# Kernel optimization log

Hardware: AMD Instinct MI355X
Metric: run time of the kernel (lower is better)

The kernel has to match this reference:

```python
import jax, jax.numpy as jnp
import numpy as np

B, F, U, O, A, H = 8192, 1024, 512, 3, 6, 4  # batch, features, nb_units, nb_opponents, actions, heads
HD = U // H  # head dim


def setup_inputs() -> dict:
    key = jax.random.key(0)
    ks = jax.random.split(key, 12)
    s = 0.02
    rn = lambda k, shape: jax.random.normal(k, shape, jnp.float32) * s
    return {
        "features": jax.random.normal(ks[0], (B, F), jnp.float32),
        # agent latent Linear
        "W_al": rn(ks[1], (U, F)), "b_al": jnp.zeros((U,), jnp.float32),
        # MultiheadAttention in_proj (q,k,v stacked) and out_proj
        "W_in": rn(ks[2], (3 * U, U)), "b_in": jnp.zeros((3 * U,), jnp.float32),
        "W_out": rn(ks[3], (U, U)), "b_out": jnp.zeros((U,), jnp.float32),
        # agent head / policy / value
        "W_ah": rn(ks[4], (U, 2 * U)), "b_ah": jnp.zeros((U,), jnp.float32),
        "W_ap": rn(ks[5], (A, U)), "b_ap": jnp.zeros((A,), jnp.float32),
        "W_av": rn(ks[6], (1, U)), "b_av": jnp.zeros((1,), jnp.float32),
        # per-opponent stacks: latent, head, policy, value
        "W_ol": rn(ks[7], (O, U, F)), "b_ol": jnp.zeros((O, U), jnp.float32),
        "W_oh": rn(ks[8], (O, U, U)), "b_oh": jnp.zeros((O, U), jnp.float32),
        "W_op": rn(ks[9], (O, A, U)), "b_op": jnp.zeros((O, A), jnp.float32),
        "W_ov": rn(ks[10], (O, 1, U)), "b_ov": jnp.zeros((O, 1), jnp.float32),
    }


def reference(features, W_al, b_al, W_in, b_in, W_out, b_out, W_ah, b_ah,
              W_ap, b_ap, W_av, b_av, W_ol, b_ol, W_oh, b_oh, W_op, b_op, W_ov, b_ov):
    elu = jax.nn.elu
    # agent + per-opponent latents (per-opponent linears as one grouped GEMM)
    agent_latent = elu(features @ W_al.T + b_al)                                # [B,U]
    opp_lat = elu(jnp.einsum('bf,ouf->obu', features, W_ol) + b_ol[:, None, :])  # [O,B,U]

    # torch.nn.MultiheadAttention: query=[1,B,U] (agent), key=value=[O,B,U] (opponents)
    Wq, Wk, Wv = W_in[:U], W_in[U:2 * U], W_in[2 * U:]
    bq, bk, bv = b_in[:U], b_in[U:2 * U], b_in[2 * U:]
    q = (agent_latent @ Wq.T + bq).reshape(B, H, HD) * (1.0 / np.sqrt(HD))      # [B,H,HD]
    k = (jnp.einsum('obu,vu->obv', opp_lat, Wk) + bk).reshape(O, B, H, HD)
    v = (jnp.einsum('obu,vu->obv', opp_lat, Wv) + bv).reshape(O, B, H, HD)
    scores = jnp.einsum('bhd,obhd->bho', q, k)                                  # [B,H,O]
    w = jax.nn.softmax(scores, axis=-1)
    attn = jnp.einsum('bho,obhd->bhd', w, v).reshape(B, U)
    attn_out = attn @ W_out.T + b_out                                           # [B,U]
    opponents_influences = w.mean(axis=1)                                       # [B,O] (avg over heads)

    # agent head / policy / value
    cat = jnp.concatenate([agent_latent, attn_out], axis=1)                     # [B,2U]
    agent_head = elu(cat @ W_ah.T + b_ah)
    agent_policy = agent_head @ W_ap.T + b_ap                                   # [B,A]
    agent_value = agent_head @ W_av.T + b_av                                    # [B,1]

    # per-opponent head / policy / value (grouped GEMMs)
    opp_heads = elu(jnp.einsum('obu,ovu->obv', opp_lat, W_oh) + b_oh[:, None, :])  # [O,B,U]
    opponents_policies = jnp.einsum('obu,oau->boa', opp_heads, W_op) + b_op[None]   # [B,O,A]
    opponents_values = jnp.einsum('obu,ocu->boc', opp_heads, W_ov) + b_ov[None]     # [B,O,1]

    return (agent_policy, agent_value, opponents_policies, opponents_values, opponents_influences)
```

## Files before the change

### kernel.cpp

```cpp
#include <hip/hip_runtime.h>

typedef unsigned short u16;
typedef __bf16 bf16x8 __attribute__((ext_vector_type(8)));
typedef float f32x4 __attribute__((ext_vector_type(4)));

#define Bsz 8192
#define Fdim 1024
#define Udim 512
#define Odim 3
#define Adim 6
#define Hdim 4

#define OFF_FEAT   0
#define OFF_WAL    8388608
#define OFF_WIN    10485760
#define OFF_WOUT   11272192
#define OFF_WAH    11534336
#define OFF_WOH    12058624
#define OFF_LAT    12845056
#define OFF_Q      29622272
#define OFF_KV     33816576
#define OFF_ATT    58982400
#define OFF_AGH    63176704
#define OFF_OPH    67371008
#define OFF_WOUTT  79953920
#define OFF_WCOMB  80216064
#define OFF_BAHC   80478208
#define OFF_ZB     80479232

#define OUT_AP 0
#define OUT_AV 49152
#define OUT_OP 57344
#define OUT_OV 204800
#define OUT_IN 229376

__device__ __forceinline__ u16 f2bf(float f) {
  return __builtin_bit_cast(u16, (__bf16)f);
}
__device__ __forceinline__ float bf2f(u16 u) {
  return (float)__builtin_bit_cast(__bf16, u);
}

__device__ __forceinline__ void gload16(const u16* g, u16* s) {
  __builtin_amdgcn_global_load_lds(
      (const __attribute__((address_space(1))) unsigned int*)g,
      (__attribute__((address_space(3))) unsigned int*)s, 16, 0, 0);
}

#define CV_E0 2097152
#define CV_E1 2228224
#define CV_E2 2621440
#define CV_E3 2818048
#define CV_E4 2883584
#define CV_E5 3014656
#define CV_E6 3211264
__global__ __launch_bounds__(256) void convert_all(
    const float* __restrict__ f, const float* __restrict__ wal,
    const float* __restrict__ wol, const float* __restrict__ win,
    const float* __restrict__ wout, const float* __restrict__ wah,
    const float* __restrict__ woh, u16* __restrict__ dst,
    u16* __restrict__ woutT, float* __restrict__ bahc,
    const float* __restrict__ bout_f, const float* __restrict__ bah_f,
    float* __restrict__ zb) {
  if (blockIdx.x >= 12608) {
    const int wave = threadIdx.x >> 6, lane = threadIdx.x & 63;
    const int jbase = (blockIdx.x - 12608) * 8 + wave * 2;
#pragma unroll
    for (int t = 0; t < 2; ++t) {
      const int j = jbase + t;
      float s = 0.f;
#pragma unroll
      for (int c = 0; c < 8; ++c)
        s += wah[j * 1024 + 512 + c * 64 + lane] * bout_f[c * 64 + lane];
#pragma unroll
      for (int d = 32; d; d >>= 1) s += __shfl_xor(s, d, 64);
      if (lane == 0) bahc[j] = bah_f[j] + s;
    }
    return;
  }
  if (blockIdx.x >= 12544) {
    const int bid = blockIdx.x - 12544;
    if (bid == 0) {
      zb[threadIdx.x] = 0.f;
      zb[threadIdx.x + 256] = 0.f;
    }
    __shared__ float tile[64][65];
    const int bx = bid & 7, byy = bid >> 3;
    const int v0 = byy * 64, u0 = bx * 64;
#pragma unroll
    for (int it = 0; it < 16; ++it) {
      int idx = it * 256 + threadIdx.x;
      int r = idx >> 6, c = idx & 63;
      tile[r][c] = wout[(v0 + r) * 512 + u0 + c];
    }
    __syncthreads();
#pragma unroll
    for (int it = 0; it < 16; ++it) {
      int idx = it * 256 + threadIdx.x;
      int r = idx >> 6, c = idx & 63;
      woutT[(u0 + r) * 512 + v0 + c] = f2bf(tile[c][r]);
    }
    return;
  }
  int i = blockIdx.x * 256 + threadIdx.x;
  const float* src;
  int base;
  if (i < CV_E0)      { src = f;    base = 0; }
  else if (i < CV_E1) { src = wal;  base = CV_E0; }
  else if (i < CV_E2) { src = wol;  base = CV_E1; }
  else if (i < CV_E3) { src = win;  base = CV_E2; }
  else if (i < CV_E4) { src = wout; base = CV_E3; }
  else if (i < CV_E5) { src = wah;  base = CV_E4; }
  else                { src = woh;  base = CV_E5; }
  float4 v = ((const float4*)src)[i - base];
  ushort4 o;
  o.x = f2bf(v.x); o.y = f2bf(v.y); o.z = f2bf(v.z); o.w = f2bf(v.w);
  ((ushort4*)dst)[i] = o;
}

#define BAR() __builtin_amdgcn_s_barrier()
#define FENCE() asm volatile("" ::: "memory")
#define LGKM0() asm volatile("s_waitcnt lgkmcnt(0)" ::: "memory")
#define VMW(n) asm volatile("s_waitcnt vmcnt(" #n ")" ::: "memory")
#define MFMA(a, b, c) __builtin_amdgcn_mfma_f32_16x16x32_bf16(a, b, c, 0, 0, 0)
#define STAGE(MAT, SRC, LD, buf, ks, kb) do {                    \
    const u16* _s = (SRC) + (size_t)(kb) + (ks) * 32;            \
    gload16(_s, &MAT[buf][ks][wave * 512]);                      \
    gload16(_s + (size_t)128 * (LD), &MAT[buf][ks][4096 + wave * 512]); \
  } while (0)
#define RD_A(cur, ks, mh) do {                                   \
    _Pragma("unroll")                                            \
    for (int mi = 0; mi < 4; mi++)                               \
      a0[mi] = *(const bf16x8*)&As[cur][ks][aoff + (mh)*2048 + mi*512]; \
  } while (0)
#define RD_B(cur, ks) do {                                       \
    _Pragma("unroll")                                            \
    for (int ni = 0; ni < 4; ni++)                               \
      b0[ni] = *(const bf16x8*)&Bs[cur][ks][boff + ni*512];      \
  } while (0)
#define MFMA8(mh) do {                                           \
    __builtin_amdgcn_s_setprio(1);                               \
    _Pragma("unroll")                                            \
    for (int mi = 0; mi < 4; mi++) {                             \
      _Pragma("unroll")                                          \
      for (int ni = 0; ni < 4; ni++)                             \
        acc[(mh)*4+mi][ni] = MFMA(a0[mi], b0[ni], acc[(mh)*4+mi][ni]); \
    }                                                            \
    __builtin_amdgcn_s_setprio(0);                               \
  } while (0)

template <bool ELU>
__global__ __launch_bounds__(512, 2) void gemm256(
    const u16* __restrict__ A, const u16* __restrict__ Bw, u16* __restrict__ C,
    const float* __restrict__ bias1, const float* __restrict__ bias2,
    int bsplit, int K, int lda, int ldb, int ldc,
    long sAz, long sBz, long sCz, int sbz, float scale) {
  __shared__ __align__(16) u16 As[2][2][8192];
  __shared__ __align__(16) u16 Bs[2][2][8192];
  const int tid = threadIdx.x;
  const int wave = tid >> 6, lane = tid & 63;
  const int wr = wave >> 2, wc = wave & 3;

  const int nx = gridDim.x, ny = gridDim.y;
  const int nxy = nx * ny;
  const int nwg = nxy * gridDim.z;
  const int orig = blockIdx.x + nx * (blockIdx.y + ny * blockIdx.z);
  const int xcd = orig & 7;
  const int qd = nwg >> 3, rd = nwg & 7;
  const int wg = (xcd < rd ? xcd * (qd + 1) : rd * (qd + 1) + (xcd - rd) * qd)
               + (orig >> 3);
  const int z = wg / nxy;
  const int rem = wg - z * nxy;
  const int by = rem / nx;
  const int bx = rem - by * nx;

  A += (size_t)z * sAz;
  Bw += (size_t)z * sBz;
  C += (size_t)z * sCz;
  bias1 += (size_t)z * sbz;

  const int tM = by * 256, tN = bx * 256;

  const int srow = tid >> 2;
  const int schunk = ((tid & 3) ^ ((tid >> 3) & 3)) * 8;
  const u16* Asrc = A + (size_t)(tM + srow) * lda + schunk;
  const u16* Bsrc = Bw + (size_t)(tN + srow) * ldb + schunk;

  const int laneLo = lane & 15;
  const int pc8 = (((lane >> 4) ^ ((lane >> 1) & 3))) * 8;
  const int aoff = (wr * 128 + laneLo) * 32 + pc8;
  const int boff = (wc * 64 + laneLo) * 32 + pc8;

  f32x4 acc[8][4];
#pragma unroll
  for (int mi = 0; mi < 8; mi++)
#pragma unroll
    for (int ni = 0; ni < 4; ni++) acc[mi][ni] = (f32x4){0.f, 0.f, 0.f, 0.f};

  const int NT = K >> 6;

  STAGE(As, Asrc, lda, 0, 0, 0);
  STAGE(Bs, Bsrc, ldb, 0, 0, 0);
  STAGE(As, Asrc, lda, 0, 1, 0);
  STAGE(Bs, Bsrc, ldb, 0, 1, 0);
  VMW(4);
  BAR();

  int cur = 0;
  int kb = 64;
  bf16x8 a0[4], b0[4];
  for (int t = 0; t < NT; ++t) {
    const int nxt = cur ^ 1;
    const bool st = (t + 1 < NT);
    RD_B(cur, 0);
    RD_A(cur, 0, 0);
    if (st) STAGE(As, Asrc, lda, nxt, 0, kb);
    FENCE(); BAR(); LGKM0();
    MFMA8(0);
    FENCE(); BAR();
    RD_A(cur, 0, 1);
    if (st) STAGE(Bs, Bsrc, ldb, nxt, 0, kb);
    FENCE(); BAR(); LGKM0();
    MFMA8(1);
    if (st) { VMW(4); } else { VMW(0); }
    BAR();
    RD_B(cur, 1);
    RD_A(cur, 1, 0);
    if (st) STAGE(As, Asrc, lda, nxt, 1, kb);
    FENCE(); BAR(); LGKM0();
    MFMA8(0);
    FENCE(); BAR();
    RD_A(cur, 1, 1);
    if (st) STAGE(Bs, Bsrc, ldb, nxt, 1, kb);
    FENCE(); BAR(); LGKM0();
    MFMA8(1);
    if (st) { VMW(4); BAR(); }
    cur = nxt;
    kb += 64;
  }

#pragma unroll
  for (int ni = 0; ni < 4; ni++) {
    const int col = tN + wc * 64 + ni * 16 + laneLo;
    const float bv = (col < bsplit) ? bias1[col] : bias2[col - bsplit];
#pragma unroll
    for (int gm = 0; gm < 8; gm++) {
      const int row0 = tM + wr * 128 + gm * 16 + (lane >> 4) * 4;
#pragma unroll
      for (int r = 0; r < 4; r++) {
        float v = (acc[gm][ni][r] + bv) * scale;
        if (ELU) v = v > 0.f ? v : (__expf(v) - 1.f);
        C[(size_t)(row0 + r) * ldc + col] = f2bf(v);
      }
    }
  }
}
#undef STAGE
#undef RD_A
#undef RD_B
#undef MFMA8

template <int BN, bool ELU>
__global__ __launch_bounds__(256) void gemm_bt(
    const u16* __restrict__ A, const u16* __restrict__ A2,
    const u16* __restrict__ Bw, const u16* __restrict__ Bw2,
    int ksplit, int lda, int lda2, int ldb, int ldb2,
    u16* __restrict__ C, const float* __restrict__ bias,
    int K, int ldc, float scale) {
  constexpr int BM = 128, BK = 32;
  constexpr int NI = BN / 32;
  __shared__ __align__(16) u16 As[BM * BK];
  __shared__ __align__(16) u16 Bs[BN * BK];
  const int wave = threadIdx.x >> 6, lane = threadIdx.x & 63;

  const int nx = gridDim.x;
  const int nwg = nx * gridDim.y;
  const int orig = blockIdx.x + nx * blockIdx.y;
  const int xcd = orig & 7;
  const int qd = nwg >> 3, rd = nwg & 7;
  const int wg = (xcd < rd ? xcd * (qd + 1) : rd * (qd + 1) + (xcd - rd) * qd)
               + (orig >> 3);
  const int by = wg / nx, bx = wg - by * nx;
  const int tM = by * BM, tN = bx * BN;
  const int wr = wave >> 1, wc = wave & 1;

  f32x4 acc[4][NI];
#pragma unroll
  for (int i = 0; i < 4; i++)
#pragma unroll
    for (int j = 0; j < NI; j++) acc[i][j] = (f32x4){0.f, 0.f, 0.f, 0.f};

  const int srow = lane >> 2;
  const int scol = (lane & 3) * 8;

  for (int k0 = 0; k0 < K; k0 += BK) {
    const u16 *Ap, *Bp;
    int la, lb, kk;
    if (k0 < ksplit) { Ap = A;  la = lda;  Bp = Bw;  lb = ldb;  kk = k0; }
    else             { Ap = A2; la = lda2; Bp = Bw2; lb = ldb2; kk = k0 - ksplit; }
    __syncthreads();
#pragma unroll
    for (int i = 0; i < 2; ++i) {
      int r = wave * 32 + i * 16;
      gload16(Ap + (size_t)(tM + r + srow) * la + kk + scol, &As[r * BK]);
    }
#pragma unroll
    for (int i = 0; i < BN / 64; ++i) {
      int r = (wave * (BN / 64) + i) * 16;
      gload16(Bp + (size_t)(tN + r + srow) * lb + kk + scol, &Bs[r * BK]);
    }
    __syncthreads();
    bf16x8 af[4], bfr[NI];
#pragma unroll
    for (int mi = 0; mi < 4; mi++)
      af[mi] = *(const bf16x8*)&As[(wr * 64 + mi * 16 + (lane & 15)) * BK + (lane >> 4) * 8];
#pragma unroll
    for (int ni = 0; ni < NI; ni++)
      bfr[ni] = *(const bf16x8*)&Bs[(wc * (BN / 2) + ni * 16 + (lane & 15)) * BK + (lane >> 4) * 8];
#pragma unroll
    for (int mi = 0; mi < 4; mi++)
#pragma unroll
      for (int ni = 0; ni < NI; ni++)
        acc[mi][ni] = __builtin_amdgcn_mfma_f32_16x16x32_bf16(af[mi], bfr[ni], acc[mi][ni], 0, 0, 0);
  }

#pragma unroll
  for (int ni = 0; ni < NI; ni++) {
    int col = tN + wc * (BN / 2) + ni * 16 + (lane & 15);
    float bv = bias[col];
#pragma unroll
    for (int mi = 0; mi < 4; mi++) {
      int row0 = tM + wr * 64 + mi * 16 + (lane >> 4) * 4;
#pragma unroll
      for (int r = 0; r < 4; r++) {
        float v = (acc[mi][ni][r] + bv) * scale;
        if (ELU) v = v > 0.f ? v : (__expf(v) - 1.f);
        C[(size_t)(row0 + r) * ldc + col] = f2bf(v);
      }
    }
  }
}

__global__ __launch_bounds__(256) void mega(
    const u16* __restrict__ lat, const u16* __restrict__ win,
    const u16* __restrict__ woh, const u16* __restrict__ wahb,
    const u16* __restrict__ woutT,
    u16* __restrict__ qb, u16* __restrict__ kvb, u16* __restrict__ oph,
    u16* __restrict__ wcomb,
    const float* __restrict__ b_in, const float* __restrict__ b_oh,
    const float* __restrict__ zb) {
  constexpr int BM = 128, BK = 32, BN = 128, NI = 4;
  __shared__ __align__(16) u16 As[BM * BK];
  __shared__ __align__(16) u16 Bs[BN * BK];
  const int wave = threadIdx.x >> 6, lane = threadIdx.x & 63;

  const int orig = blockIdx.x;
  const int wg = (orig & 7) * 322 + (orig >> 3);

  const u16 *A, *Bw;
  u16* C;
  const float* bias;
  int bx, by, ldc, lda = 2048;
  bool elu = false;
  float scale = 1.f;
  if (wg < 256) {
    bx = wg & 3; by = wg >> 2;
    A = lat; Bw = win; C = qb; bias = b_in;
    ldc = 512; scale = 0.08838834764831845f;
  } else if (wg < 1792) {
    int t = wg - 256, o = t >> 9, r = t & 511;
    bx = r & 7; by = r >> 3;
    A = lat + 512 * (o + 1); Bw = win + 262144;
    C = kvb + (size_t)o * 8388608; bias = b_in + 512;
    ldc = 1024;
  } else if (wg < 2560) {
    int t = wg - 1792, o = t >> 8, r = t & 255;
    bx = r & 3; by = r >> 2;
    A = lat + 512 * (o + 1); Bw = woh + (size_t)o * 262144;
    C = oph + (size_t)o * 4194304; bias = b_oh + o * 512;
    ldc = 512; elu = true;
  } else {
    int t = wg - 2560;
    bx = t & 3; by = t >> 2;
    A = wahb + 512; lda = 1024; Bw = woutT;
    C = wcomb; bias = zb;
    ldc = 512;
  }
  const int tM = by * BM, tN = bx * BN;
  const int wr = wave >> 1, wc = wave & 1;

  f32x4 acc[4][NI];
#pragma unroll
  for (int i = 0; i < 4; i++)
#pragma unroll
    for (int j = 0; j < NI; j++) acc[i][j] = (f32x4){0.f, 0.f, 0.f, 0.f};

  const int srow = lane >> 2;
  const int scol = (lane & 3) * 8;

  for (int k0 = 0; k0 < 512; k0 += BK) {
    __syncthreads();
#pragma unroll
    for (int i = 0; i < 2; ++i) {
      int r = wave * 32 + i * 16;
      gload16(A + (size_t)(tM + r + srow) * lda + k0 + scol, &As[r * BK]);
    }
#pragma unroll
    for (int i = 0; i < 2; ++i) {
      int r = (wave * 2 + i) * 16;
      gload16(Bw + (size_t)(tN + r + srow) * 512 + k0 + scol, &Bs[r * BK]);
    }
    __syncthreads();
    bf16x8 af[4], bfr[NI];
#pragma unroll
    for (int mi = 0; mi < 4; mi++)
      af[mi] = *(const bf16x8*)&As[(wr * 64 + mi * 16 + (lane & 15)) * BK + (lane >> 4) * 8];
#pragma unroll
    for (int ni = 0; ni < NI; ni++)
      bfr[ni] = *(const bf16x8*)&Bs[(wc * 64 + ni * 16 + (lane & 15)) * BK + (lane >> 4) * 8];
#pragma unroll
    for (int mi = 0; mi < 4; mi++)
#pragma unroll
      for (int ni = 0; ni < NI; ni++)
        acc[mi][ni] = __builtin_amdgcn_mfma_f32_16x16x32_bf16(af[mi], bfr[ni], acc[mi][ni], 0, 0, 0);
  }

#pragma unroll
  for (int ni = 0; ni < NI; ni++) {
    int col = tN + wc * 64 + ni * 16 + (lane & 15);
    float bv = bias[col];
#pragma unroll
    for (int mi = 0; mi < 4; mi++) {
      int row0 = tM + wr * 64 + mi * 16 + (lane >> 4) * 4;
#pragma unroll
      for (int r = 0; r < 4; r++) {
        float v = (acc[mi][ni][r] + bv) * scale;
        if (elu) v = v > 0.f ? v : (__expf(v) - 1.f);
        C[(size_t)(row0 + r) * ldc + col] = f2bf(v);
      }
    }
  }
}

__global__ __launch_bounds__(256) void attn_kernel(
    const u16* __restrict__ q, const u16* __restrict__ kv,
    u16* __restrict__ attn, float* __restrict__ influ) {
  const int wave = threadIdx.x >> 6, lane = threadIdx.x & 63;
  const int b = blockIdx.x * 4 + wave;
  const size_t qb = (size_t)b * 512;
  float wacc0 = 0.f, wacc1 = 0.f, wacc2 = 0.f;
#pragma unroll
  for (int h = 0; h < 4; ++h) {
    const int off = h * 128 + lane * 2;
    ushort2 qu = *(const ushort2*)(q + qb + off);
    float qx = bf2f(qu.x), qy = bf2f(qu.y);
    float s[3];
#pragma unroll
    for (int o = 0; o < 3; ++o) {
      ushort2 ku = *(const ushort2*)(kv + (size_t)o * (Bsz * 1024) + (size_t)b * 1024 + off);
      float p = qx * bf2f(ku.x) + qy * bf2f(ku.y);
#pragma unroll
      for (int d = 32; d; d >>= 1) p += __shfl_xor(p, d, 64);
      s[o] = p;
    }
    float m = fmaxf(s[0], fmaxf(s[1], s[2]));
    float e0 = __expf(s[0] - m), e1 = __expf(s[1] - m), e2 = __expf(s[2] - m);
    float inv = 1.f / (e0 + e1 + e2);
    float w0 = e0 * inv, w1 = e1 * inv, w2 = e2 * inv;
    wacc0 += w0; wacc1 += w1; wacc2 += w2;
    float ax = 0.f, ay = 0.f;
#pragma unroll
    for (int o = 0; o < 3; ++o) {
      float w = (o == 0) ? w0 : (o == 1) ? w1 : w2;
      ushort2 vu = *(const ushort2*)(kv + (size_t)o * (Bsz * 1024) + (size_t)b * 1024 + 512 + off);
      ax += w * bf2f(vu.x);
      ay += w * bf2f(vu.y);
    }
    ushort2 st; st.x = f2bf(ax); st.y = f2bf(ay);
    *(ushort2*)(attn + qb + off) = st;
  }
  if (lane == 0) {
    influ[b * 3 + 0] = wacc0 * 0.25f;
    influ[b * 3 + 1] = wacc1 * 0.25f;
    influ[b * 3 + 2] = wacc2 * 0.25f;
  }
}

__global__ __launch_bounds__(256) void heads_kernel(
    const u16* __restrict__ ah, const u16* __restrict__ oh,
    const float* __restrict__ Wap, const float* __restrict__ bap,
    const float* __restrict__ Wav, const float* __restrict__ bav,
    const float* __restrict__ Wop, const float* __restrict__ bop,
    const float* __restrict__ Wov, const float* __restrict__ bov,
    float* __restrict__ out) {
  __shared__ float sW[14336];
  for (int i = threadIdx.x; i < 14336; i += 256) {
    int s = i / 3584, rem = i - s * 3584;
    float v;
    if (s == 0) {
      v = (rem < 3072) ? Wap[rem] : Wav[rem - 3072];
    } else {
      int o = s - 1;
      v = (rem < 3072) ? Wop[o * 3072 + rem] : Wov[o * 512 + (rem - 3072)];
    }
    sW[i] = v;
  }
  __syncthreads();
  const int wave = threadIdx.x >> 6, lane = threadIdx.x & 63;
  const int kq = lane & 7, r = lane >> 3;
  const int b = blockIdx.x * 32 + wave * 8 + r;

  const u16* srcs[4] = {ah + (size_t)b * 512,
                        oh + (size_t)b * 512,
                        oh + (size_t)(Bsz + b) * 512,
                        oh + (size_t)(2 * Bsz + b) * 512};
  bf16x8 a[4][8];
#pragma unroll
  for (int s = 0; s < 4; s++)
#pragma unroll
    for (int c = 0; c < 8; c++)
      a[s][c] = *(const bf16x8*)(srcs[s] + c * 64 + kq * 8);

#pragma unroll
  for (int s = 0; s < 4; s++) {
#pragma unroll
    for (int p = 0; p < 7; p++) {
      const float* w = &sW[s * 3584 + p * 512 + kq * 8];
      float acc = 0.f;
#pragma unroll
      for (int c = 0; c < 8; c++) {
#pragma unroll
        for (int j = 0; j < 8; j++)
          acc += (float)a[s][c][j] * w[c * 64 + j];
      }
      acc += __shfl_xor(acc, 1, 64);
      acc += __shfl_xor(acc, 2, 64);
      acc += __shfl_xor(acc, 4, 64);
      if (kq == p) {
        if (s == 0) {
          if (p < 6) out[OUT_AP + b * 6 + p] = acc + bap[p];
          else       out[OUT_AV + b] = acc + bav[0];
        } else {
          int o = s - 1;
          if (p < 6) out[OUT_OP + b * 18 + o * 6 + p] = acc + bop[o * 6 + p];
          else       out[OUT_OV + b * 3 + o] = acc + bov[o];
        }
      }
    }
  }
}

extern "C" void kernel_launch(void* const* d_in, const int* in_sizes, int n_in,
                              void* d_out, int out_size, void* d_ws, size_t ws_size,
                              hipStream_t stream) {
  (void)in_sizes; (void)n_in; (void)out_size; (void)ws_size;
  const float* f     = (const float*)d_in[0];
  const float* W_al  = (const float*)d_in[1];
  const float* b_al  = (const float*)d_in[2];
  const float* W_in  = (const float*)d_in[3];
  const float* b_in  = (const float*)d_in[4];
  const float* W_out = (const float*)d_in[5];
  const float* b_out = (const float*)d_in[6];
  const float* W_ah  = (const float*)d_in[7];
  const float* b_ah  = (const float*)d_in[8];
  const float* W_ap  = (const float*)d_in[9];
  const float* b_ap  = (const float*)d_in[10];
  const float* W_av  = (const float*)d_in[11];
  const float* b_av  = (const float*)d_in[12];
  const float* W_ol  = (const float*)d_in[13];
  const float* b_ol  = (const float*)d_in[14];
  const float* W_oh  = (const float*)d_in[15];
  const float* b_oh  = (const float*)d_in[16];
  const float* W_op  = (const float*)d_in[17];
  const float* b_op  = (const float*)d_in[18];
  const float* W_ov  = (const float*)d_in[19];
  const float* b_ov  = (const float*)d_in[20];
  float* out = (float*)d_out;
  u16* ws = (u16*)d_ws;

  u16* feat  = ws + OFF_FEAT;
  u16* wal   = ws + OFF_WAL;
  u16* win   = ws + OFF_WIN;
  u16* wahb  = ws + OFF_WAH;
  u16* woh   = ws + OFF_WOH;
  u16* lat   = ws + OFF_LAT;
  u16* qb    = ws + OFF_Q;
  u16* kvb   = ws + OFF_KV;
  u16* att   = ws + OFF_ATT;
  u16* agh   = ws + OFF_AGH;
  u16* oph   = ws + OFF_OPH;
  u16* woutT = ws + OFF_WOUTT;
  u16* wcomb = ws + OFF_WCOMB;
  float* bahc = (float*)(ws + OFF_BAHC);
  float* zb   = (float*)(ws + OFF_ZB);

  convert_all<<<12672, 256, 0, stream>>>(f, W_al, W_ol, W_in, W_out, W_ah,
                                         W_oh, ws, woutT, bahc, b_out, b_ah,
                                         zb);

  gemm256<true><<<dim3(8, 32, 1), 512, 0, stream>>>(
      feat, wal, lat, b_al, b_ol, 512, 1024, 1024, 1024, 2048, 0, 0, 0, 0, 1.f);

  mega<<<2576, 256, 0, stream>>>(
      lat, win, woh, wahb, woutT, qb, kvb, oph, wcomb, b_in, b_oh, zb);

  attn_kernel<<<2048, 256, 0, stream>>>(qb, kvb, att, out + OUT_IN);

  gemm_bt<64, true><<<dim3(8, 64), 256, 0, stream>>>(
      lat, att, wahb, wcomb, 512, 2048, 512, 1024, 512,
      agh, bahc, 1024, 512, 1.f);

  heads_kernel<<<256, 256, 0, stream>>>(agh, oph, W_ap, b_ap, W_av, b_av,
                                        W_op, b_op, W_ov, b_ov, out);
}
```

Baseline: 290.9 us.

## Fuse attention, agent-head GEMM and policy/value heads into one tail kernel

Replaces the attention kernel, the agent-head GEMM and the heads kernel with a single tail kernel that handles 32 batch rows per 512-thread block. Attention output and agent latent stay in swizzled LDS, and the agent head result is written back to LDS and consumed directly by the policy/value dot products. This drops the global round trips for the attn and agent_head buffers and two kernel launches. In exchange only 256 blocks run, each with a serial 32-step K loop and no double buffering. Head weights are read from global fp32 instead of being staged in LDS.

```diff
diff --git a/kernel.cpp b/kernel.cpp
--- a/kernel.cpp
+++ b/kernel.cpp
@@ -20,8 +20,6 @@
 #define OFF_LAT    12845056
 #define OFF_Q      29622272
 #define OFF_KV     33816576
-#define OFF_ATT    58982400
-#define OFF_AGH    63176704
 #define OFF_OPH    67371008
 #define OFF_WOUTT  79953920
 #define OFF_WCOMB  80216064
@@ -260,87 +258,6 @@
 #undef RD_B
 #undef MFMA8
 
-template <int BN, bool ELU>
-__global__ __launch_bounds__(256) void gemm_bt(
-    const u16* __restrict__ A, const u16* __restrict__ A2,
-    const u16* __restrict__ Bw, const u16* __restrict__ Bw2,
-    int ksplit, int lda, int lda2, int ldb, int ldb2,
-    u16* __restrict__ C, const float* __restrict__ bias,
-    int K, int ldc, float scale) {
-  constexpr int BM = 128, BK = 32;
-  constexpr int NI = BN / 32;
-  __shared__ __align__(16) u16 As[BM * BK];
-  __shared__ __align__(16) u16 Bs[BN * BK];
-  const int wave = threadIdx.x >> 6, lane = threadIdx.x & 63;
-
-  const int nx = gridDim.x;
-  const int nwg = nx * gridDim.y;
-  const int orig = blockIdx.x + nx * blockIdx.y;
-  const int xcd = orig & 7;
-  const int qd = nwg >> 3, rd = nwg & 7;
-  const int wg = (xcd < rd ? xcd * (qd + 1) : rd * (qd + 1) + (xcd - rd) * qd)
-               + (orig >> 3);
-  const int by = wg / nx, bx = wg - by * nx;
-  const int tM = by * BM, tN = bx * BN;
-  const int wr = wave >> 1, wc = wave & 1;
-
-  f32x4 acc[4][NI];
-#pragma unroll
-  for (int i = 0; i < 4; i++)
-#pragma unroll
-    for (int j = 0; j < NI; j++) acc[i][j] = (f32x4){0.f, 0.f, 0.f, 0.f};
-
-  const int srow = lane >> 2;
-  const int scol = (lane & 3) * 8;
-
-  for (int k0 = 0; k0 < K; k0 += BK) {
-    const u16 *Ap, *Bp;
-    int la, lb, kk;
-    if (k0 < ksplit) { Ap = A;  la = lda;  Bp = Bw;  lb = ldb;  kk = k0; }
-    else             { Ap = A2; la = lda2; Bp = Bw2; lb = ldb2; kk = k0 - ksplit; }
-    __syncthreads();
-#pragma unroll
-    for (int i = 0; i < 2; ++i) {
-      int r = wave * 32 + i * 16;
-      gload16(Ap + (size_t)(tM + r + srow) * la + kk + scol, &As[r * BK]);
-    }
-#pragma unroll
-    for (int i = 0; i < BN / 64; ++i) {
-      int r = (wave * (BN / 64) + i) * 16;
-      gload16(Bp + (size_t)(tN + r + srow) * lb + kk + scol, &Bs[r * BK]);
-    }
-    __syncthreads();
-    bf16x8 af[4], bfr[NI];
-#pragma unroll
-    for (int mi = 0; mi < 4; mi++)
-      af[mi] = *(const bf16x8*)&As[(wr * 64 + mi * 16 + (lane & 15)) * BK + (lane >> 4) * 8];
-#pragma unroll
-    for (int ni = 0; ni < NI; ni++)
-      bfr[ni] = *(const bf16x8*)&Bs[(wc * (BN / 2) + ni * 16 + (lane & 15)) * BK + (lane >> 4) * 8];
-#pragma unroll
-    for (int mi = 0; mi < 4; mi++)
-#pragma unroll
-      for (int ni = 0; ni < NI; ni++)
-        acc[mi][ni] = __builtin_amdgcn_mfma_f32_16x16x32_bf16(af[mi], bfr[ni], acc[mi][ni], 0, 0, 0);
-  }
-
-#pragma unroll
-  for (int ni = 0; ni < NI; ni++) {
-    int col = tN + wc * (BN / 2) + ni * 16 + (lane & 15);
-    float bv = bias[col];
-#pragma unroll
-    for (int mi = 0; mi < 4; mi++) {
-      int row0 = tM + wr * 64 + mi * 16 + (lane >> 4) * 4;
-#pragma unroll
-      for (int r = 0; r < 4; r++) {
-        float v = (acc[mi][ni][r] + bv) * scale;
-        if (ELU) v = v > 0.f ? v : (__expf(v) - 1.f);
-        C[(size_t)(row0 + r) * ldc + col] = f2bf(v);
-      }
-    }
-  }
-}
-
 __global__ __launch_bounds__(256) void mega(
     const u16* __restrict__ lat, const u16* __restrict__ win,
     const u16* __restrict__ woh, const u16* __restrict__ wahb,
@@ -442,108 +359,176 @@
   }
 }
 
-__global__ __launch_bounds__(256) void attn_kernel(
-    const u16* __restrict__ q, const u16* __restrict__ kv,
-    u16* __restrict__ attn, float* __restrict__ influ) {
-  const int wave = threadIdx.x >> 6, lane = threadIdx.x & 63;
-  const int b = blockIdx.x * 4 + wave;
-  const size_t qb = (size_t)b * 512;
-  float wacc0 = 0.f, wacc1 = 0.f, wacc2 = 0.f;
-#pragma unroll
-  for (int h = 0; h < 4; ++h) {
-    const int off = h * 128 + lane * 2;
-    ushort2 qu = *(const ushort2*)(q + qb + off);
-    float qx = bf2f(qu.x), qy = bf2f(qu.y);
-    float s[3];
-#pragma unroll
-    for (int o = 0; o < 3; ++o) {
-      ushort2 ku = *(const ushort2*)(kv + (size_t)o * (Bsz * 1024) + (size_t)b * 1024 + off);
-      float p = qx * bf2f(ku.x) + qy * bf2f(ku.y);
-#pragma unroll
-      for (int d = 32; d; d >>= 1) p += __shfl_xor(p, d, 64);
-      s[o] = p;
-    }
-    float m = fmaxf(s[0], fmaxf(s[1], s[2]));
-    float e0 = __expf(s[0] - m), e1 = __expf(s[1] - m), e2 = __expf(s[2] - m);
-    float inv = 1.f / (e0 + e1 + e2);
-    float w0 = e0 * inv, w1 = e1 * inv, w2 = e2 * inv;
-    wacc0 += w0; wacc1 += w1; wacc2 += w2;
-    float ax = 0.f, ay = 0.f;
-#pragma unroll
-    for (int o = 0; o < 3; ++o) {
-      float w = (o == 0) ? w0 : (o == 1) ? w1 : w2;
-      ushort2 vu = *(const ushort2*)(kv + (size_t)o * (Bsz * 1024) + (size_t)b * 1024 + 512 + off);
-      ax += w * bf2f(vu.x);
-      ay += w * bf2f(vu.y);
-    }
-    ushort2 st; st.x = f2bf(ax); st.y = f2bf(ay);
-    *(ushort2*)(attn + qb + off) = st;
-  }
-  if (lane == 0) {
-    influ[b * 3 + 0] = wacc0 * 0.25f;
-    influ[b * 3 + 1] = wacc1 * 0.25f;
-    influ[b * 3 + 2] = wacc2 * 0.25f;
-  }
-}
-
-__global__ __launch_bounds__(256) void heads_kernel(
-    const u16* __restrict__ ah, const u16* __restrict__ oh,
+__global__ __launch_bounds__(512) void tail(
+    const u16* __restrict__ lat, const u16* __restrict__ qb,
+    const u16* __restrict__ kvb, const u16* __restrict__ wahb,
+    const u16* __restrict__ wcomb, const float* __restrict__ bahc,
+    const u16* __restrict__ oph,
     const float* __restrict__ Wap, const float* __restrict__ bap,
     const float* __restrict__ Wav, const float* __restrict__ bav,
     const float* __restrict__ Wop, const float* __restrict__ bop,
     const float* __restrict__ Wov, const float* __restrict__ bov,
     float* __restrict__ out) {
-  __shared__ float sW[14336];
-  for (int i = threadIdx.x; i < 14336; i += 256) {
-    int s = i / 3584, rem = i - s * 3584;
-    float v;
-    if (s == 0) {
-      v = (rem < 3072) ? Wap[rem] : Wav[rem - 3072];
-    } else {
-      int o = s - 1;
-      v = (rem < 3072) ? Wop[o * 3072 + rem] : Wov[o * 512 + (rem - 3072)];
-    }
-    sW[i] = v;
+  __shared__ __align__(16) u16 AL[16384];
+  __shared__ __align__(16) u16 ATT[16384];
+  __shared__ __align__(16) u16 Bs[16384];
+  const int tid = threadIdx.x;
+  const int wave = tid >> 6, lane = tid & 63;
+  const int row0 = blockIdx.x * 32;
+
+#pragma unroll
+  for (int j = 0; j < 4; ++j) {
+    int gq = j * 512 + tid;
+    int r = gq >> 6, s = gq & 63, c = s ^ (r & 7);
+    gload16(lat + (size_t)(row0 + r) * 2048 + c * 8, &AL[j * 4096 + wave * 512]);
+  }
+
+  for (int t = 0; t < 4; ++t) {
+    const int b = row0 + wave * 4 + t;
+    const int rl = b - row0;
+    const size_t qoff = (size_t)b * 512;
+    float wacc0 = 0.f, wacc1 = 0.f, wacc2 = 0.f;
+#pragma unroll
+    for (int h = 0; h < 4; ++h) {
+      const int off = h * 128 + lane * 2;
+      ushort2 qu = *(const ushort2*)(qb + qoff + off);
+      float qx = bf2f(qu.x), qy = bf2f(qu.y);
+      float s[3];
+#pragma unroll
+      for (int o = 0; o < 3; ++o) {
+        ushort2 ku = *(const ushort2*)(kvb + (size_t)o * (Bsz * 1024) + (size_t)b * 1024 + off);
+        float p = qx * bf2f(ku.x) + qy * bf2f(ku.y);
+#pragma unroll
+        for (int d = 32; d; d >>= 1) p += __shfl_xor(p, d, 64);
+        s[o] = p;
+      }
+      float m = fmaxf(s[0], fmaxf(s[1], s[2]));
+      float e0 = __expf(s[0] - m), e1 = __expf(s[1] - m), e2 = __expf(s[2] - m);
+      float inv = 1.f / (e0 + e1 + e2);
+      float w0 = e0 * inv, w1 = e1 * inv, w2 = e2 * inv;
+      wacc0 += w0; wacc1 += w1; wacc2 += w2;
+      float ax = 0.f, ay = 0.f;
+#pragma unroll
+      for (int o = 0; o < 3; ++o) {
+        float w = (o == 0) ? w0 : (o == 1) ? w1 : w2;
+        ushort2 vu = *(const ushort2*)(kvb + (size_t)o * (Bsz * 1024) + (size_t)b * 1024 + 512 + off);
+        ax += w * bf2f(vu.x);
+        ay += w * bf2f(vu.y);
+      }
+      ushort2 st; st.x = f2bf(ax); st.y = f2bf(ay);
+      const int col = off;
+      const int slot = (col >> 3) ^ (rl & 7);
+      *(ushort2*)(&ATT[rl * 512 + slot * 8 + (col & 7)]) = st;
+    }
+    if (lane == 0) {
+      out[OUT_IN + (size_t)b * 3 + 0] = wacc0 * 0.25f;
+      out[OUT_IN + (size_t)b * 3 + 1] = wacc1 * 0.25f;
+      out[OUT_IN + (size_t)b * 3 + 2] = wacc2 * 0.25f;
+    }
   }
   __syncthreads();
-  const int wave = threadIdx.x >> 6, lane = threadIdx.x & 63;
-  const int kq = lane & 7, r = lane >> 3;
-  const int b = blockIdx.x * 32 + wave * 8 + r;
-
-  const u16* srcs[4] = {ah + (size_t)b * 512,
-                        oh + (size_t)b * 512,
-                        oh + (size_t)(Bsz + b) * 512,
-                        oh + (size_t)(2 * Bsz + b) * 512};
-  bf16x8 a[4][8];
-#pragma unroll
-  for (int s = 0; s < 4; s++)
-#pragma unroll
-    for (int c = 0; c < 8; c++)
-      a[s][c] = *(const bf16x8*)(srcs[s] + c * 64 + kq * 8);
-
-#pragma unroll
-  for (int s = 0; s < 4; s++) {
-#pragma unroll
-    for (int p = 0; p < 7; p++) {
-      const float* w = &sW[s * 3584 + p * 512 + kq * 8];
-      float acc = 0.f;
-#pragma unroll
-      for (int c = 0; c < 8; c++) {
-#pragma unroll
-        for (int j = 0; j < 8; j++)
-          acc += (float)a[s][c][j] * w[c * 64 + j];
-      }
-      acc += __shfl_xor(acc, 1, 64);
-      acc += __shfl_xor(acc, 2, 64);
-      acc += __shfl_xor(acc, 4, 64);
+
+  const int ll = lane & 15, lh = lane >> 4, l7 = lane & 7;
+  const int wc0 = wave * 64;
+  f32x4 acc[2][4];
+#pragma unroll
+  for (int mf = 0; mf < 2; ++mf)
+#pragma unroll
+    for (int nf = 0; nf < 4; ++nf) acc[mf][nf] = (f32x4){0.f, 0.f, 0.f, 0.f};
+
+  for (int step = 0; step < 32; ++step) {
+    const u16* bsrc;
+    int ldb;
+    if (step < 16) { bsrc = wahb + step * 32;          ldb = 1024; }
+    else           { bsrc = wcomb + (step - 16) * 32;  ldb = 512; }
+    __syncthreads();
+#pragma unroll
+    for (int j = 0; j < 4; ++j) {
+      int id = j * 512 + tid;
+      gload16(bsrc + (size_t)(id >> 2) * ldb + (id & 3) * 8,
+              &Bs[j * 4096 + wave * 512]);
+    }
+    __syncthreads();
+    const u16* ABUF = (step < 16) ? AL : ATT;
+    const int c9 = step & 15;
+    bf16x8 a0 = *(const bf16x8*)&ABUF[ll * 512 + (((c9 * 4 + lh) ^ l7) * 8)];
+    bf16x8 a1 = *(const bf16x8*)&ABUF[(16 + ll) * 512 + (((c9 * 4 + lh) ^ l7) * 8)];
+#pragma unroll
+    for (int nf = 0; nf < 4; ++nf) {
+      bf16x8 bf = *(const bf16x8*)&Bs[(wc0 + nf * 16 + ll) * 32 + lh * 8];
+      acc[0][nf] = __builtin_amdgcn_mfma_f32_16x16x32_bf16(a0, bf, acc[0][nf], 0, 0, 0);
+      acc[1][nf] = __builtin_amdgcn_mfma_f32_16x16x32_bf16(a1, bf, acc[1][nf], 0, 0, 0);
+    }
+  }
+
+#pragma unroll
+  for (int nf = 0; nf < 4; ++nf) {
+    const int col = wc0 + nf * 16 + ll;
+    const float bb = bahc[col];
+#pragma unroll
+    for (int mf = 0; mf < 2; ++mf)
+#pragma unroll
+      for (int r = 0; r < 4; ++r) {
+        const int row = mf * 16 + lh * 4 + r;
+        float v = acc[mf][nf][r] + bb;
+        v = v > 0.f ? v : (__expf(v) - 1.f);
+        AL[row * 512 + (((col >> 3) ^ (row & 7)) * 8) + (col & 7)] = f2bf(v);
+      }
+  }
+  __syncthreads();
+
+  if (wave < 4) {
+    const int rl = wave * 8 + (lane >> 3), kq = lane & 7;
+    const int b = row0 + rl;
+    bf16x8 av[8];
+#pragma unroll
+    for (int c = 0; c < 8; ++c)
+      av[c] = *(const bf16x8*)&AL[rl * 512 + (((c * 8 + kq) ^ (rl & 7)) * 8)];
+#pragma unroll
+    for (int p = 0; p < 7; ++p) {
+      const float* wg = (p < 6) ? Wap + p * 512 : Wav;
+      float ac = 0.f;
+#pragma unroll
+      for (int c = 0; c < 8; ++c) {
+        float4 w0 = *(const float4*)(wg + c * 64 + kq * 8);
+        float4 w1 = *(const float4*)(wg + c * 64 + kq * 8 + 4);
+        ac += (float)av[c][0] * w0.x + (float)av[c][1] * w0.y
+            + (float)av[c][2] * w0.z + (float)av[c][3] * w0.w
+            + (float)av[c][4] * w1.x + (float)av[c][5] * w1.y
+            + (float)av[c][6] * w1.z + (float)av[c][7] * w1.w;
+      }
+      ac += __shfl_xor(ac, 1, 64);
+      ac += __shfl_xor(ac, 2, 64);
+      ac += __shfl_xor(ac, 4, 64);
       if (kq == p) {
-        if (s == 0) {
-          if (p < 6) out[OUT_AP + b * 6 + p] = acc + bap[p];
-          else       out[OUT_AV + b] = acc + bav[0];
-        } else {
-          int o = s - 1;
-          if (p < 6) out[OUT_OP + b * 18 + o * 6 + p] = acc + bop[o * 6 + p];
-          else       out[OUT_OV + b * 3 + o] = acc + bov[o];
+        if (p < 6) out[OUT_AP + b * 6 + p] = ac + bap[p];
+        else       out[OUT_AV + b] = ac + bav[0];
+      }
+    }
+    for (int o = 0; o < 3; ++o) {
+      const u16* src = oph + ((size_t)o * Bsz + b) * 512;
+#pragma unroll
+      for (int c = 0; c < 8; ++c)
+        av[c] = *(const bf16x8*)(src + c * 64 + kq * 8);
+#pragma unroll
+      for (int p = 0; p < 7; ++p) {
+        const float* wg = (p < 6) ? Wop + o * 3072 + p * 512 : Wov + o * 512;
+        float ac = 0.f;
+#pragma unroll
+        for (int c = 0; c < 8; ++c) {
+          float4 w0 = *(const float4*)(wg + c * 64 + kq * 8);
+          float4 w1 = *(const float4*)(wg + c * 64 + kq * 8 + 4);
+          ac += (float)av[c][0] * w0.x + (float)av[c][1] * w0.y
+              + (float)av[c][2] * w0.z + (float)av[c][3] * w0.w
+              + (float)av[c][4] * w1.x + (float)av[c][5] * w1.y
+              + (float)av[c][6] * w1.z + (float)av[c][7] * w1.w;
+        }
+        ac += __shfl_xor(ac, 1, 64);
+        ac += __shfl_xor(ac, 2, 64);
+        ac += __shfl_xor(ac, 4, 64);
+        if (kq == p) {
+          if (p < 6) out[OUT_OP + b * 18 + o * 6 + p] = ac + bop[o * 6 + p];
+          else       out[OUT_OV + b * 3 + o] = ac + bov[o];
         }
       }
     }
@@ -584,10 +569,8 @@
   u16* wahb  = ws + OFF_WAH;
   u16* woh   = ws + OFF_WOH;
   u16* lat   = ws + OFF_LAT;
-  u16* qb    = ws + OFF_Q;
+  u16* qbuf  = ws + OFF_Q;
   u16* kvb   = ws + OFF_KV;
-  u16* att   = ws + OFF_ATT;
-  u16* agh   = ws + OFF_AGH;
   u16* oph   = ws + OFF_OPH;
   u16* woutT = ws + OFF_WOUTT;
   u16* wcomb = ws + OFF_WCOMB;
@@ -602,14 +585,9 @@
       feat, wal, lat, b_al, b_ol, 512, 1024, 1024, 1024, 2048, 0, 0, 0, 0, 1.f);
 
   mega<<<2576, 256, 0, stream>>>(
-      lat, win, woh, wahb, woutT, qb, kvb, oph, wcomb, b_in, b_oh, zb);
-
-  attn_kernel<<<2048, 256, 0, stream>>>(qb, kvb, att, out + OUT_IN);
-
-  gemm_bt<64, true><<<dim3(8, 64), 256, 0, stream>>>(
-      lat, att, wahb, wcomb, 512, 2048, 512, 1024, 512,
-      agh, bahc, 1024, 512, 1.f);
-
-  heads_kernel<<<256, 256, 0, stream>>>(agh, oph, W_ap, b_ap, W_av, b_av,
-                                        W_op, b_op, W_ov, b_ov, out);
-}
+      lat, win, woh, wahb, woutT, qbuf, kvb, oph, wcomb, b_in, b_oh, zb);
+
+  tail<<<256, 512, 0, stream>>>(lat, qbuf, kvb, wahb, wcomb, bahc, oph,
+                                W_ap, b_ap, W_av, b_av,
+                                W_op, b_op, W_ov, b_ov, out);
+}
```

Result: no change. 291.4 us (+0.2%).
